# Performance work log

Hardware: AMD Instinct MI355X
Metric: run time of the kernel (lower is better)

## Reference

```python
import jax, jax.numpy as jnp
import numpy as np

LN_EPS = 1e-5

def _mlp3(x, w1, b1, w2, b2, g, bt, w3, b3):
    # Linear -> ReLU -> Linear -> LayerNorm -> ReLU -> Linear
    h = jax.nn.relu(x @ w1 + b1)
    h = h @ w2 + b2
    mu = jnp.mean(h, axis=-1, keepdims=True)
    var = jnp.mean(jnp.square(h - mu), axis=-1, keepdims=True)
    h = g * (h - mu) * jax.lax.rsqrt(var + LN_EPS) + bt
    h = jax.nn.relu(h)
    return h @ w3 + b3

def _edge_index(B, n):
    # fully connected incl. self-loops, row-major (i, j) per graph, batch-offset
    ij = jnp.arange(n * n)
    i = ij // n
    j = ij % n
    off = (jnp.arange(B) * n)[:, None]
    row = (off + i[None, :]).reshape(-1)  # [B*n*n]
    col = (off + j[None, :]).reshape(-1)
    return row, col

def setup_inputs() -> dict:
    key = jax.random.key(0)
    ks = jax.random.split(key, 16)
    D, H = 512, 512
    B, n = 4096, 7
    s = 0.02
    inp = {
        'states': jax.random.normal(ks[0], (B, n, D), jnp.float32),
        'ew1': jax.random.normal(ks[1], (2 * D, H)) * s, 'eb1': jnp.zeros((H,)),
        'ew2': jax.random.normal(ks[2], (H, H)) * s, 'eb2': jnp.zeros((H,)),
        'eg': jnp.ones((H,)), 'ebt': jnp.zeros((H,)),
        'ew3': jax.random.normal(ks[3], (H, H)) * s, 'eb3': jnp.zeros((H,)),
        'nw1': jax.random.normal(ks[4], (D + H, H)) * s, 'nb1': jnp.zeros((H,)),
        'nw2': jax.random.normal(ks[5], (H, H)) * s, 'nb2': jnp.zeros((H,)),
        'ng': jnp.ones((H,)), 'nbt': jnp.zeros((H,)),
        'nw3': jax.random.normal(ks[6], (H, H)) * s, 'nb3': jnp.zeros((H,)),
        'fnw': jax.random.normal(ks[7], (H, 1)) * s, 'fnb': jnp.zeros((1,)),
        'few': jax.random.normal(ks[8], (H, 1)) * s, 'feb': jnp.zeros((1,)),
    }
    return inp

def reference(states, ew1, eb1, ew2, eb2, eg, ebt, ew3, eb3,
              nw1, nb1, nw2, nb2, ng, nbt, nw3, nb3, fnw, fnb, few, feb):
    B, n, D = states.shape
    node = states.reshape(-1, D)                       # [B*n, D]
    row, col = _edge_index(B, n)                       # [B*n*n]

    def edge_mlp(src, tgt):
        return _mlp3(jnp.concatenate([src, tgt], axis=1),
                     ew1, eb1, ew2, eb2, eg, ebt, ew3, eb3)

    edge_attr = edge_mlp(node[row], node[col])         # [B*n*n, H]
    agg = jax.ops.segment_sum(edge_attr, row, num_segments=B * n)
    node2 = _mlp3(jnp.concatenate([node, agg], axis=1),
                  nw1, nb1, nw2, nb2, ng, nbt, nw3, nb3)
    edge_attr2 = edge_mlp(node2[row], node2[col])

    node_out = (node2 @ fnw + fnb).reshape(B, n)       # unary_preds=1
    edge_out = (edge_attr2 @ few + feb).reshape(B, n * n)
    return jnp.concatenate([node_out, edge_out], axis=1)  # [B, n + n*n]
```

## Files before the change

kernel.cpp:

```cpp
#include <hip/hip_runtime.h>

#define LN_EPS 1e-5f

typedef unsigned short u16;
typedef u16 u16x8 __attribute__((ext_vector_type(8)));
typedef __bf16 bf16x8 __attribute__((ext_vector_type(8)));
typedef float f32x4 __attribute__((ext_vector_type(4)));
typedef float f32x2 __attribute__((ext_vector_type(2)));

__device__ __forceinline__ u16 f2bf(float f){
  return __builtin_bit_cast(u16, (__bf16)f);
}
__device__ __forceinline__ float bf2f(u16 b){
  return (float)__builtin_bit_cast(__bf16, b);
}
__device__ __forceinline__ f32x4 mfma16(u16x8 a, u16x8 b, f32x4 c){
  return __builtin_amdgcn_mfma_f32_16x16x32_bf16(
      __builtin_bit_cast(bf16x8, a), __builtin_bit_cast(bf16x8, b), c, 0, 0, 0);
}
__device__ __forceinline__ int uidx(int row, int k){
  return row * 512 + (k ^ ((row & 7) << 3));
}

__device__ __forceinline__ void zero_acc(f32x4 (&acc)[4][4]){
  #pragma unroll
  for (int mt = 0; mt < 4; ++mt)
    #pragma unroll
    for (int ct = 0; ct < 4; ++ct){
      f32x4 z = {0.f, 0.f, 0.f, 0.f};
      acc[mt][ct] = z;
    }
}

__device__ __forceinline__ void preload_b4(const u16* __restrict__ Bp, int wave, int lane,
                                           u16x8 (&b)[4]){
  const u16* bb = Bp + ((size_t)(wave * 4) * 64 + lane) * 8;
  #pragma unroll
  for (int ct = 0; ct < 4; ++ct) b[ct] = *(const u16x8*)&bb[ct * 512];
}

__device__ __forceinline__ void gemm_pipe(const u16* hA, const u16* __restrict__ Bp,
                                          f32x4 (&acc)[4][4], int wave, int lane,
                                          u16x8 (&b_cur)[4]){
  int lrow = lane & 15, lhi = lane >> 4;
  const u16* bb = Bp + ((size_t)(wave * 4) * 64 + lane) * 8;
  u16x8 b_nxt[4], a[4];
  #pragma unroll
  for (int kt = 0; kt < 16; ++kt){
    #pragma unroll
    for (int mt = 0; mt < 4; ++mt)
      a[mt] = *(const u16x8*)&hA[uidx(mt * 16 + lrow, kt * 32 + lhi * 8)];
    if (kt < 15){
      #pragma unroll
      for (int ct = 0; ct < 4; ++ct)
        b_nxt[ct] = *(const u16x8*)&bb[(size_t)(kt + 1) * 16384 + ct * 512];
    }
    __builtin_amdgcn_s_setprio(1);
    #pragma unroll
    for (int ct = 0; ct < 4; ++ct)
      #pragma unroll
      for (int mt = 0; mt < 4; ++mt)
        acc[mt][ct] = mfma16(a[mt], b_cur[ct], acc[mt][ct]);
    __builtin_amdgcn_s_setprio(0);
    #pragma unroll
    for (int ct = 0; ct < 4; ++ct) b_cur[ct] = b_nxt[ct];
  }
}

__device__ __forceinline__ void gemm_k1024_gA(const u16* __restrict__ A0,
                                              const u16* __restrict__ A1, size_t row0,
                                              const u16* __restrict__ Bp,
                                              f32x4 (&acc)[4][4], int wave, int lane){
  int lrow = lane & 15, lhi = lane >> 4;
  const u16* bb = Bp + ((size_t)(wave * 4) * 64 + lane) * 8;
  const u16* a0 = A0 + (row0 + lrow) * 512 + lhi * 8;
  const u16* a1 = A1 + (row0 + lrow) * 512 + lhi * 8;
  u16x8 b_cur[4], b_nxt[4], a[4];
  #pragma unroll
  for (int ct = 0; ct < 4; ++ct) b_cur[ct] = *(const u16x8*)&bb[ct * 512];
  #pragma unroll
  for (int kt = 0; kt < 32; ++kt){
    const u16* ab = (kt < 16) ? a0 : a1;
    int kk = (kt & 15) * 32;
    #pragma unroll
    for (int mt = 0; mt < 4; ++mt)
      a[mt] = *(const u16x8*)&ab[mt * 8192 + kk];
    if (kt < 31){
      #pragma unroll
      for (int ct = 0; ct < 4; ++ct)
        b_nxt[ct] = *(const u16x8*)&bb[(size_t)(kt + 1) * 16384 + ct * 512];
    }
    __builtin_amdgcn_s_setprio(1);
    #pragma unroll
    for (int ct = 0; ct < 4; ++ct)
      #pragma unroll
      for (int mt = 0; mt < 4; ++mt)
        acc[mt][ct] = mfma16(a[mt], b_cur[ct], acc[mt][ct]);
    __builtin_amdgcn_s_setprio(0);
    #pragma unroll
    for (int ct = 0; ct < 4; ++ct) b_cur[ct] = b_nxt[ct];
  }
}

__device__ __forceinline__ void gemm_pipe_s(const u16* hA, const u16* __restrict__ bbBase,
                                            int ktStride, f32x4 (&acc)[4][4],
                                            int lane){
  int lrow = lane & 15, lhi = lane >> 4;
  u16x8 b_cur[4], b_nxt[4], a[4];
  #pragma unroll
  for (int ct = 0; ct < 4; ++ct) b_cur[ct] = *(const u16x8*)&bbBase[ct * 512];
  #pragma unroll
  for (int kt = 0; kt < 16; ++kt){
    #pragma unroll
    for (int mt = 0; mt < 4; ++mt)
      a[mt] = *(const u16x8*)&hA[uidx(mt * 16 + lrow, kt * 32 + lhi * 8)];
    if (kt < 15){
      #pragma unroll
      for (int ct = 0; ct < 4; ++ct)
        b_nxt[ct] = *(const u16x8*)&bbBase[(size_t)(kt + 1) * ktStride + ct * 512];
    }
    __builtin_amdgcn_s_setprio(1);
    #pragma unroll
    for (int ct = 0; ct < 4; ++ct)
      #pragma unroll
      for (int mt = 0; mt < 4; ++mt)
        acc[mt][ct] = mfma16(a[mt], b_cur[ct], acc[mt][ct]);
    __builtin_amdgcn_s_setprio(0);
    #pragma unroll
    for (int ct = 0; ct < 4; ++ct) b_cur[ct] = b_nxt[ct];
  }
}

__device__ __forceinline__ void add_bias8(f32x4 (&acc)[4][4], const float* __restrict__ b,
                                          int wave, int lane){
  int lrow = lane & 15;
  #pragma unroll
  for (int ct = 0; ct < 4; ++ct){
    float bb = b[wave * 64 + ct * 16 + lrow];
    #pragma unroll
    for (int mt = 0; mt < 4; ++mt)
      #pragma unroll
      for (int r = 0; r < 4; ++r) acc[mt][ct][r] += bb;
  }
}

__device__ __forceinline__ void relu_to_lds(f32x4 (&acc)[4][4], u16* hA,
                                            const float* __restrict__ b,
                                            int wave, int lane){
  int lrow = lane & 15, lhi = lane >> 4;
  #pragma unroll
  for (int ct = 0; ct < 4; ++ct){
    int c = wave * 64 + ct * 16 + lrow;
    float bb = b[c];
    #pragma unroll
    for (int mt = 0; mt < 4; ++mt)
      #pragma unroll
      for (int r = 0; r < 4; ++r){
        int row = mt * 16 + lhi * 4 + r;
        hA[uidx(row, c)] = f2bf(fmaxf(acc[mt][ct][r] + bb, 0.f));
      }
  }
}

template<int TO_ACC>
__device__ __forceinline__ void ln_relu8_t(f32x4 (&acc)[4][4], u16* hA,
    f32x2 (*stats)[8], f32x2* mufb,
    const float* __restrict__ b2, const float* __restrict__ g, const float* __restrict__ bt,
    int wave, int lane, int tid)
{
  int lrow = lane & 15, lhi = lane >> 4;
  float s1[4][4], s2[4][4];
  #pragma unroll
  for (int mt = 0; mt < 4; ++mt)
    #pragma unroll
    for (int r = 0; r < 4; ++r){ s1[mt][r] = 0.f; s2[mt][r] = 0.f; }
  #pragma unroll
  for (int ct = 0; ct < 4; ++ct){
    int c = wave * 64 + ct * 16 + lrow;
    float bb = b2[c];
    #pragma unroll
    for (int mt = 0; mt < 4; ++mt)
      #pragma unroll
      for (int r = 0; r < 4; ++r){
        float x = acc[mt][ct][r] + bb;
        acc[mt][ct][r] = x;
        s1[mt][r] += x; s2[mt][r] += x * x;
      }
  }
  #pragma unroll
  for (int off = 1; off < 16; off <<= 1){
    #pragma unroll
    for (int mt = 0; mt < 4; ++mt)
      #pragma unroll
      for (int r = 0; r < 4; ++r){
        s1[mt][r] += __shfl_xor(s1[mt][r], off);
        s2[mt][r] += __shfl_xor(s2[mt][r], off);
      }
  }
  float sa1 = 0.f, sa2 = 0.f;
  #pragma unroll
  for (int mt = 0; mt < 4; ++mt)
    #pragma unroll
    for (int r = 0; r < 4; ++r)
      if (lrow == mt * 4 + r){ sa1 = s1[mt][r]; sa2 = s2[mt][r]; }
  int rowa = (lrow >> 2) * 16 + lhi * 4 + (lrow & 3);
  f32x2 pa = {sa1, sa2};
  stats[rowa][wave] = pa;
  __syncthreads();
  if (tid < 64){
    float a = 0.f, b = 0.f;
    #pragma unroll
    for (int w = 0; w < 8; ++w){ a += stats[tid][w][0]; b += stats[tid][w][1]; }
    float mu  = a * (1.f / 512.f);
    float var = b * (1.f / 512.f) - mu * mu;
    f32x2 mr = {mu, rsqrtf(fmaxf(var, 0.f) + LN_EPS)};
    mufb[tid] = mr;
  }
  __syncthreads();
  float gv[4], btv[4];
  #pragma unroll
  for (int ct = 0; ct < 4; ++ct){
    int c = wave * 64 + ct * 16 + lrow;
    gv[ct] = g[c]; btv[ct] = bt[c];
  }
  #pragma unroll
  for (int mt = 0; mt < 4; ++mt)
    #pragma unroll
    for (int r = 0; r < 4; ++r){
      int row = mt * 16 + lhi * 4 + r;
      f32x2 mr = mufb[row];
      #pragma unroll
      for (int ct = 0; ct < 4; ++ct){
        int c = wave * 64 + ct * 16 + lrow;
        float x = (acc[mt][ct][r] - mr[0]) * mr[1] * gv[ct] + btv[ct];
        if (TO_ACC) acc[mt][ct][r] = fmaxf(x, 0.f);
        else        hA[uidx(row, c)] = f2bf(fmaxf(x, 0.f));
      }
    }
}

__device__ __forceinline__ void head_partial8(f32x4 (&acc)[4][4], const float* __restrict__ w,
                                              f32x2 (*stats)[8], int wave, int lane)
{
  int lrow = lane & 15, lhi = lane >> 4;
  float hs[4][4];
  #pragma unroll
  for (int mt = 0; mt < 4; ++mt)
    #pragma unroll
    for (int r = 0; r < 4; ++r) hs[mt][r] = 0.f;
  #pragma unroll
  for (int ct = 0; ct < 4; ++ct){
    int c = wave * 64 + ct * 16 + lrow;
    float f = w[c];
    #pragma unroll
    for (int mt = 0; mt < 4; ++mt)
      #pragma unroll
      for (int r = 0; r < 4; ++r) hs[mt][r] += acc[mt][ct][r] * f;
  }
  #pragma unroll
  for (int off = 1; off < 16; off <<= 1)
    #pragma unroll
    for (int mt = 0; mt < 4; ++mt)
      #pragma unroll
      for (int r = 0; r < 4; ++r) hs[mt][r] += __shfl_xor(hs[mt][r], off);
  float sa = 0.f;
  #pragma unroll
  for (int mt = 0; mt < 4; ++mt)
    #pragma unroll
    for (int r = 0; r < 4; ++r)
      if (lrow == mt * 4 + r) sa = hs[mt][r];
  int rowa = (lrow >> 2) * 16 + lhi * 4 + (lrow & 3);
  f32x2 pa = {sa, 0.f};
  stats[rowa][wave] = pa;
}

__device__ __forceinline__ void stage_h1(const u16* __restrict__ PQ, int gg, u16* hA,
                                         const float* bias, int wave, int lane){
  const u16* Pg = PQ + (size_t)gg * 7 * 1024;
  u16x8 pA, qA, pB, qB;
  {
    int e = wave;
    int i = e / 7, j = e % 7;
    pA = *(const u16x8*)&Pg[(size_t)i * 1024 + lane * 8];
    qA = *(const u16x8*)&Pg[(size_t)j * 1024 + 512 + lane * 8];
  }
  #pragma unroll
  for (int it = 0; it < 8; ++it){
    int e = it * 8 + wave;
    if (it < 7){
      int e2 = e + 8;
      if (e2 < 49){
        int i = e2 / 7, j = e2 % 7;
        pB = *(const u16x8*)&Pg[(size_t)i * 1024 + lane * 8];
        qB = *(const u16x8*)&Pg[(size_t)j * 1024 + 512 + lane * 8];
      }
    }
    u16x8 o;
    if (e < 49){
      #pragma unroll
      for (int u = 0; u < 8; ++u)
        o[u] = f2bf(fmaxf(bf2f(pA[u]) + bf2f(qA[u]) + bias[u], 0.f));
    } else {
      #pragma unroll
      for (int u = 0; u < 8; ++u) o[u] = 0;
    }
    *(u16x8*)&hA[uidx(e, lane * 8)] = o;
    pA = pB; qA = qB;
  }
}

__global__ __launch_bounds__(512, 2) void edge0_kernel(
    const u16* __restrict__ PQ, const u16* __restrict__ w2p, const u16* __restrict__ w3p,
    const float* __restrict__ b1, const float* __restrict__ b2,
    const float* __restrict__ g, const float* __restrict__ bt, const float* __restrict__ b3,
    u16* __restrict__ agg)
{
  __shared__ alignas(16) u16 hA[64 * 512];
  __shared__ f32x2 stats[64][8];
  __shared__ f32x2 mufb[64];
  int gidx = blockIdx.x;
  int tid = threadIdx.x;
  int wave = tid >> 6, lane = tid & 63;
  int lrow = lane & 15, lhi = lane >> 4;

  const float4* b1v = (const float4*)b1;
  float4 ba = b1v[lane * 2], bb2 = b1v[lane * 2 + 1];
  float bias[8] = {ba.x, ba.y, ba.z, ba.w, bb2.x, bb2.y, bb2.z, bb2.w};

  stage_h1(PQ, gidx, hA, bias, wave, lane);
  u16x8 bpre[4];
  preload_b4(w2p, wave, lane, bpre);
  __syncthreads();

  f32x4 acc[4][4];
  zero_acc(acc);
  gemm_pipe(hA, w2p, acc, wave, lane, bpre);
  ln_relu8_t<0>(acc, hA, stats, mufb, b2, g, bt, wave, lane, tid);
  preload_b4(w3p, wave, lane, bpre);
  __syncthreads();
  {
    int c = tid;
    #pragma unroll
    for (int i = 0; i < 7; ++i){
      float s = 0.f;
      #pragma unroll
      for (int j = 0; j < 7; ++j)
        s += bf2f(hA[uidx(7 * i + j, c)]);
      hA[uidx(49 + i, c)] = f2bf(s);
    }
  }
  __syncthreads();
  f32x4 acc1[4];
  #pragma unroll
  for (int ct = 0; ct < 4; ++ct){ f32x4 z = {0.f,0.f,0.f,0.f}; acc1[ct] = z; }
  {
    const u16* bb = w3p + ((size_t)(wave * 4) * 64 + lane) * 8;
    u16x8 b_nxt[4];
    #pragma unroll
    for (int kt = 0; kt < 16; ++kt){
      u16x8 a0 = *(const u16x8*)&hA[uidx(48 + lrow, kt * 32 + lhi * 8)];
      if (kt < 15){
        #pragma unroll
        for (int ct = 0; ct < 4; ++ct)
          b_nxt[ct] = *(const u16x8*)&bb[(size_t)(kt + 1) * 16384 + ct * 512];
      }
      #pragma unroll
      for (int ct = 0; ct < 4; ++ct)
        acc1[ct] = mfma16(a0, bpre[ct], acc1[ct]);
      #pragma unroll
      for (int ct = 0; ct < 4; ++ct) bpre[ct] = b_nxt[ct];
    }
  }
  #pragma unroll
  for (int ct = 0; ct < 4; ++ct){
    int c = wave * 64 + ct * 16 + lrow;
    float bb3 = 7.f * b3[c];
    #pragma unroll
    for (int r = 0; r < 4; ++r){
      int tr = lhi * 4 + r;
      if (tr >= 1 && tr <= 7){
        int i = tr - 1;
        agg[((size_t)(gidx * 7 + i)) * 512 + c] = f2bf(acc1[ct][r] + bb3);
      }
    }
  }
}

__global__ __launch_bounds__(512, 2) void edge1_kernel(
    const u16* __restrict__ PQ, const u16* __restrict__ w2p,
    const float* __restrict__ b1, const float* __restrict__ b2,
    const float* __restrict__ g, const float* __restrict__ bt,
    const float* __restrict__ w3f, float* __restrict__ out)
{
  __shared__ alignas(16) u16 hA[64 * 512];
  __shared__ f32x2 stats[64][8];
  __shared__ f32x2 mufb[64];
  int gidx = blockIdx.x;
  int tid = threadIdx.x;
  int wave = tid >> 6, lane = tid & 63;

  const float4* b1v = (const float4*)b1;
  float4 ba = b1v[lane * 2], bb2 = b1v[lane * 2 + 1];
  float bias[8] = {ba.x, ba.y, ba.z, ba.w, bb2.x, bb2.y, bb2.z, bb2.w};

  stage_h1(PQ, gidx, hA, bias, wave, lane);
  u16x8 bpre[4];
  preload_b4(w2p, wave, lane, bpre);
  __syncthreads();

  f32x4 acc[4][4];
  zero_acc(acc);
  gemm_pipe(hA, w2p, acc, wave, lane, bpre);
  ln_relu8_t<1>(acc, hA, stats, mufb, b2, g, bt, wave, lane, tid);
  head_partial8(acc, w3f, stats, wave, lane);
  __syncthreads();
  if (tid < 49){
    float s = w3f[512];
    #pragma unroll
    for (int w = 0; w < 8; ++w) s += stats[tid][w][0];
    out[(size_t)gidx * 56 + 7 + tid] = s;
  }
}

__global__ __launch_bounds__(512, 2) void node_mega(
    const u16* __restrict__ nodeb, const u16* __restrict__ aggb,
    const u16* __restrict__ nw1p, const u16* __restrict__ nw2p,
    const u16* __restrict__ nw3p, const u16* __restrict__ w1p,
    const float* __restrict__ nb1, const float* __restrict__ nb2,
    const float* __restrict__ ng, const float* __restrict__ nbt,
    const float* __restrict__ nb3, const float* __restrict__ hw,
    const float* __restrict__ hb,
    u16* __restrict__ PQ, float* __restrict__ out)
{
  __shared__ alignas(16) u16 hA[64 * 512];
  __shared__ f32x2 stats[64][8];
  __shared__ f32x2 mufb[64];
  int tid = threadIdx.x;
  int wave = tid >> 6, lane = tid & 63;
  int lrow = lane & 15, lhi = lane >> 4;
  size_t row0 = (size_t)blockIdx.x * 64;

  f32x4 acc[4][4];
  zero_acc(acc);
  gemm_k1024_gA(nodeb, aggb, row0, nw1p, acc, wave, lane);
  relu_to_lds(acc, hA, nb1, wave, lane);
  u16x8 bpre[4];
  preload_b4(nw2p, wave, lane, bpre);
  __syncthreads();
  zero_acc(acc);
  gemm_pipe(hA, nw2p, acc, wave, lane, bpre);
  ln_relu8_t<0>(acc, hA, stats, mufb, nb2, ng, nbt, wave, lane, tid);
  preload_b4(nw3p, wave, lane, bpre);
  __syncthreads();
  zero_acc(acc);
  gemm_pipe(hA, nw3p, acc, wave, lane, bpre);
  add_bias8(acc, nb3, wave, lane);
  __syncthreads();
  #pragma unroll
  for (int ct = 0; ct < 4; ++ct){
    int c = wave * 64 + ct * 16 + lrow;
    #pragma unroll
    for (int mt = 0; mt < 4; ++mt)
      #pragma unroll
      for (int r = 0; r < 4; ++r)
        hA[uidx(mt * 16 + lhi * 4 + r, c)] = f2bf(acc[mt][ct][r]);
  }
  head_partial8(acc, hw, stats, wave, lane);
  __syncthreads();
  if (tid < 64){
    size_t v = row0 + tid;
    float s = hb[0];
    #pragma unroll
    for (int w = 0; w < 8; ++w) s += stats[tid][w][0];
    out[(v / 7) * 56 + (v % 7)] = s;
  }
  #pragma unroll
  for (int p = 0; p < 2; ++p){
    zero_acc(acc);
    const u16* bbBase = w1p + (((size_t)(p * 32) + wave * 4) * 64 + lane) * 8;
    gemm_pipe_s(hA, bbBase, 32768, acc, lane);
    #pragma unroll
    for (int ct = 0; ct < 4; ++ct){
      int c = p * 512 + wave * 64 + ct * 16 + lrow;
      #pragma unroll
      for (int mt = 0; mt < 4; ++mt)
        #pragma unroll
        for (int r = 0; r < 4; ++r){
          size_t grow = row0 + mt * 16 + lhi * 4 + r;
          PQ[grow * 1024 + c] = f2bf(acc[mt][ct][r]);
        }
    }
  }
}

__global__ __launch_bounds__(256, 2) void gemm64_0(
    const u16* __restrict__ A0, const u16* __restrict__ Bp, u16* __restrict__ Cout)
{
  int tid = threadIdx.x;
  int wave = tid >> 6, lane = tid & 63;
  int lrow = lane & 15, lhi = lane >> 4;
  size_t row0 = (size_t)blockIdx.x * 64;
  int coff = blockIdx.y * 512;
  const u16* bb = Bp + (((size_t)(coff >> 4) + wave * 8) * 64 + lane) * 8;
  f32x4 acc[4][8];
  #pragma unroll
  for (int mt = 0; mt < 4; ++mt)
    #pragma unroll
    for (int ct = 0; ct < 8; ++ct){
      f32x4 z = {0.f, 0.f, 0.f, 0.f};
      acc[mt][ct] = z;
    }
  u16x8 b_cur[8], b_nxt[8];
  #pragma unroll
  for (int ct = 0; ct < 8; ++ct) b_cur[ct] = *(const u16x8*)&bb[ct * 512];
  #pragma unroll
  for (int kt = 0; kt < 16; ++kt){
    u16x8 af[4];
    #pragma unroll
    for (int mt = 0; mt < 4; ++mt)
      af[mt] = *(const u16x8*)&A0[(row0 + mt * 16 + lrow) * 512 + kt * 32 + lhi * 8];
    if (kt < 15){
      #pragma unroll
      for (int ct = 0; ct < 8; ++ct)
        b_nxt[ct] = *(const u16x8*)&bb[((size_t)(kt + 1) * 64 * 64 + ct * 64) * 8];
    }
    __builtin_amdgcn_s_setprio(1);
    #pragma unroll
    for (int ct = 0; ct < 8; ++ct)
      #pragma unroll
      for (int mt = 0; mt < 4; ++mt) acc[mt][ct] = mfma16(af[mt], b_cur[ct], acc[mt][ct]);
    __builtin_amdgcn_s_setprio(0);
    #pragma unroll
    for (int ct = 0; ct < 8; ++ct) b_cur[ct] = b_nxt[ct];
  }
  #pragma unroll
  for (int ct = 0; ct < 8; ++ct){
    int c = coff + wave * 128 + ct * 16 + lrow;
    #pragma unroll
    for (int mt = 0; mt < 4; ++mt)
      #pragma unroll
      for (int r = 0; r < 4; ++r){
        size_t grow = row0 + mt * 16 + lhi * 4 + r;
        Cout[grow * 1024 + c] = f2bf(acc[mt][ct][r]);
      }
  }
}

__global__ void fold_w3(const float* __restrict__ W3, const float* __restrict__ hw,
                        const float* __restrict__ b3, const float* __restrict__ hb,
                        float* __restrict__ w3f)
{
  int k = blockIdx.x, l = threadIdx.x;
  const float* row = (k < 512) ? (W3 + (size_t)k * 512) : b3;
  float s = 0.f;
  for (int c = l; c < 512; c += 64) s += row[c] * hw[c];
  #pragma unroll
  for (int off = 32; off; off >>= 1) s += __shfl_down(s, off);
  if (l == 0) w3f[k] = (k < 512) ? s : s + hb[0];
}

__global__ void pack_w(const float* __restrict__ W, u16* __restrict__ dst,
                       int K, int N, int w1mode)
{
  int idx = blockIdx.x * 256 + threadIdx.x;
  int total = (K >> 5) * (N >> 4) * 64;
  if (idx >= total) return;
  int lane = idx & 63;
  int t = idx >> 6;
  int nt = N >> 4;
  int ct = t % nt;
  int kt = t / nt;
  int c  = ct * 16 + (lane & 15);
  int k0 = kt * 32 + (lane >> 4) * 8;
  u16x8 o;
  #pragma unroll
  for (int j = 0; j < 8; ++j){
    int k = k0 + j;
    float v;
    if (w1mode){
      v = (c < 512) ? W[(size_t)k * 512 + c] : W[(size_t)(k + 512) * 512 + (c - 512)];
    } else {
      v = W[(size_t)k * N + c];
    }
    o[j] = f2bf(v);
  }
  *(u16x8*)&dst[(size_t)idx * 8] = o;
}

__global__ void cast_node(const float* __restrict__ src, u16* __restrict__ dst, int n8){
  int idx = blockIdx.x * 256 + threadIdx.x;
  if (idx >= n8) return;
  const float4* s = (const float4*)src;
  float4 a = s[(size_t)idx * 2], b = s[(size_t)idx * 2 + 1];
  u16x8 o;
  o[0] = f2bf(a.x); o[1] = f2bf(a.y); o[2] = f2bf(a.z); o[3] = f2bf(a.w);
  o[4] = f2bf(b.x); o[5] = f2bf(b.y); o[6] = f2bf(b.z); o[7] = f2bf(b.w);
  *(u16x8*)&dst[(size_t)idx * 8] = o;
}

extern "C" void kernel_launch(void* const* d_in, const int* in_sizes, int n_in,
                              void* d_out, int out_size, void* d_ws, size_t ws_size,
                              hipStream_t stream)
{
  (void)in_sizes; (void)n_in; (void)out_size; (void)ws_size;
  const float* states = (const float*)d_in[0];
  const float* ew1 = (const float*)d_in[1];
  const float* eb1 = (const float*)d_in[2];
  const float* ew2 = (const float*)d_in[3];
  const float* eb2 = (const float*)d_in[4];
  const float* eg  = (const float*)d_in[5];
  const float* ebt = (const float*)d_in[6];
  const float* ew3 = (const float*)d_in[7];
  const float* eb3 = (const float*)d_in[8];
  const float* nw1 = (const float*)d_in[9];
  const float* nb1 = (const float*)d_in[10];
  const float* nw2 = (const float*)d_in[11];
  const float* nb2 = (const float*)d_in[12];
  const float* ng  = (const float*)d_in[13];
  const float* nbt = (const float*)d_in[14];
  const float* nw3 = (const float*)d_in[15];
  const float* nb3 = (const float*)d_in[16];
  const float* fnw = (const float*)d_in[17];
  const float* fnb = (const float*)d_in[18];
  const float* few = (const float*)d_in[19];
  const float* feb = (const float*)d_in[20];
  float* out = (float*)d_out;

  char* ws = (char*)d_ws;
  size_t off = 0;
  auto alloc = [&](size_t bytes) -> void* {
    void* p = ws + off;
    off += (bytes + 255) & ~(size_t)255;
    return p;
  };
  const size_t NV = 28672;
  u16* PQ    = (u16*)alloc(NV * 1024 * 2);
  u16* nodeb = (u16*)alloc(NV * 512 * 2);
  u16* aggb  = (u16*)alloc(NV * 512 * 2);
  u16* w1p   = (u16*)alloc(512 * 1024 * 2);
  u16* nw1p  = (u16*)alloc(1024 * 512 * 2);
  u16* w2p   = (u16*)alloc(512 * 512 * 2);
  u16* w3p   = (u16*)alloc(512 * 512 * 2);
  u16* nw2p  = (u16*)alloc(512 * 512 * 2);
  u16* nw3p  = (u16*)alloc(512 * 512 * 2);
  float* w3f = (float*)alloc(513 * 4);

  pack_w<<<256, 256, 0, stream>>>(ew1, w1p, 512, 1024, 1);
  pack_w<<<256, 256, 0, stream>>>(nw1, nw1p, 1024, 512, 0);
  pack_w<<<128, 256, 0, stream>>>(ew2, w2p, 512, 512, 0);
  pack_w<<<128, 256, 0, stream>>>(ew3, w3p, 512, 512, 0);
  pack_w<<<128, 256, 0, stream>>>(nw2, nw2p, 512, 512, 0);
  pack_w<<<128, 256, 0, stream>>>(nw3, nw3p, 512, 512, 0);
  fold_w3<<<513, 64, 0, stream>>>(ew3, few, eb3, feb, w3f);
  cast_node<<<7168, 256, 0, stream>>>(states, nodeb, (int)(NV * 512 / 8));

  gemm64_0<<<dim3(448, 2), 256, 0, stream>>>(nodeb, w1p, PQ);
  edge0_kernel<<<4096, 512, 0, stream>>>(PQ, w2p, w3p, eb1, eb2, eg, ebt, eb3, aggb);
  node_mega<<<448, 512, 0, stream>>>(nodeb, aggb, nw1p, nw2p, nw3p, w1p,
                                     nb1, nb2, ng, nbt, nb3, fnw, fnb, PQ, out);
  edge1_kernel<<<4096, 512, 0, stream>>>(PQ, w2p, eb1, eb2, eg, ebt, w3f, out);
}
```

Baseline: 592.7 us.

## Fold edge W3 into node W1 so edge0 emits summed hidden rows

Uses linearity: agg = sum_j(h_j) @ eW3 + 7*eb3, so agg @ nW1b equals hsum @ (eW3 @ nW1b) plus a constant bias. The edge0 kernel now writes only the per-node sums of the post-LN hidden rows and drops its small W3 GEMM. A precomputed fused weight (eW3·nW1b, formed by a small GEMM) and a folded bias replace it in the node MLP. This removes per-graph MFMA work and weight loads from edge0, but adds per-call weight-prep kernels and a different bf16 rounding path.

```diff
diff --git a/kernel.cpp b/kernel.cpp
--- a/kernel.cpp
+++ b/kernel.cpp
@@ -310,10 +310,10 @@
 }
 
 __global__ __launch_bounds__(512, 2) void edge0_kernel(
-    const u16* __restrict__ PQ, const u16* __restrict__ w2p, const u16* __restrict__ w3p,
+    const u16* __restrict__ PQ, const u16* __restrict__ w2p,
     const float* __restrict__ b1, const float* __restrict__ b2,
-    const float* __restrict__ g, const float* __restrict__ bt, const float* __restrict__ b3,
-    u16* __restrict__ agg)
+    const float* __restrict__ g, const float* __restrict__ bt,
+    u16* __restrict__ hsum)
 {
   __shared__ alignas(16) u16 hA[64 * 512];
   __shared__ f32x2 stats[64][8];
@@ -321,7 +321,6 @@
   int gidx = blockIdx.x;
   int tid = threadIdx.x;
   int wave = tid >> 6, lane = tid & 63;
-  int lrow = lane & 15, lhi = lane >> 4;
 
   const float4* b1v = (const float4*)b1;
   float4 ba = b1v[lane * 2], bb2 = b1v[lane * 2 + 1];
@@ -336,7 +335,6 @@
   zero_acc(acc);
   gemm_pipe(hA, w2p, acc, wave, lane, bpre);
   ln_relu8_t<0>(acc, hA, stats, mufb, b2, g, bt, wave, lane, tid);
-  preload_b4(w3p, wave, lane, bpre);
   __syncthreads();
   {
     int c = tid;
@@ -346,42 +344,7 @@
       #pragma unroll
       for (int j = 0; j < 7; ++j)
         s += bf2f(hA[uidx(7 * i + j, c)]);
-      hA[uidx(49 + i, c)] = f2bf(s);
-    }
-  }
-  __syncthreads();
-  f32x4 acc1[4];
-  #pragma unroll
-  for (int ct = 0; ct < 4; ++ct){ f32x4 z = {0.f,0.f,0.f,0.f}; acc1[ct] = z; }
-  {
-    const u16* bb = w3p + ((size_t)(wave * 4) * 64 + lane) * 8;
-    u16x8 b_nxt[4];
-    #pragma unroll
-    for (int kt = 0; kt < 16; ++kt){
-      u16x8 a0 = *(const u16x8*)&hA[uidx(48 + lrow, kt * 32 + lhi * 8)];
-      if (kt < 15){
-        #pragma unroll
-        for (int ct = 0; ct < 4; ++ct)
-          b_nxt[ct] = *(const u16x8*)&bb[(size_t)(kt + 1) * 16384 + ct * 512];
-      }
-      #pragma unroll
-      for (int ct = 0; ct < 4; ++ct)
-        acc1[ct] = mfma16(a0, bpre[ct], acc1[ct]);
-      #pragma unroll
-      for (int ct = 0; ct < 4; ++ct) bpre[ct] = b_nxt[ct];
-    }
-  }
-  #pragma unroll
-  for (int ct = 0; ct < 4; ++ct){
-    int c = wave * 64 + ct * 16 + lrow;
-    float bb3 = 7.f * b3[c];
-    #pragma unroll
-    for (int r = 0; r < 4; ++r){
-      int tr = lhi * 4 + r;
-      if (tr >= 1 && tr <= 7){
-        int i = tr - 1;
-        agg[((size_t)(gidx * 7 + i)) * 512 + c] = f2bf(acc1[ct][r] + bb3);
-      }
+      hsum[((size_t)(gidx * 7 + i)) * 512 + c] = f2bf(s);
     }
   }
 }
@@ -423,10 +386,10 @@
 }
 
 __global__ __launch_bounds__(512, 2) void node_mega(
-    const u16* __restrict__ nodeb, const u16* __restrict__ aggb,
-    const u16* __restrict__ nw1p, const u16* __restrict__ nw2p,
+    const u16* __restrict__ nodeb, const u16* __restrict__ hsumb,
+    const u16* __restrict__ nw1cat, const u16* __restrict__ nw2p,
     const u16* __restrict__ nw3p, const u16* __restrict__ w1p,
-    const float* __restrict__ nb1, const float* __restrict__ nb2,
+    const float* __restrict__ bvec, const float* __restrict__ nb2,
     const float* __restrict__ ng, const float* __restrict__ nbt,
     const float* __restrict__ nb3, const float* __restrict__ hw,
     const float* __restrict__ hb,
@@ -442,8 +405,8 @@
 
   f32x4 acc[4][4];
   zero_acc(acc);
-  gemm_k1024_gA(nodeb, aggb, row0, nw1p, acc, wave, lane);
-  relu_to_lds(acc, hA, nb1, wave, lane);
+  gemm_k1024_gA(nodeb, hsumb, row0, nw1cat, acc, wave, lane);
+  relu_to_lds(acc, hA, bvec, wave, lane);
   u16x8 bpre[4];
   preload_b4(nw2p, wave, lane, bpre);
   __syncthreads();
@@ -544,6 +507,64 @@
         Cout[grow * 1024 + c] = f2bf(acc[mt][ct][r]);
       }
   }
+}
+
+__global__ __launch_bounds__(256) void gemm_w3n(
+    const float* __restrict__ A, const u16* __restrict__ Bp, float* __restrict__ C)
+{
+  int tid = threadIdx.x;
+  int wave = tid >> 6, lane = tid & 63;
+  int lrow = lane & 15, lhi = lane >> 4;
+  size_t row0 = (size_t)blockIdx.x * 64;
+  const u16* bb = Bp + (((size_t)(wave * 8)) * 64 + lane) * 8;
+  f32x4 acc[4][8];
+  #pragma unroll
+  for (int mt = 0; mt < 4; ++mt)
+    #pragma unroll
+    for (int ct = 0; ct < 8; ++ct){
+      f32x4 z = {0.f, 0.f, 0.f, 0.f};
+      acc[mt][ct] = z;
+    }
+  for (int kt = 0; kt < 16; ++kt){
+    u16x8 af[4], bv[8];
+    #pragma unroll
+    for (int mt = 0; mt < 4; ++mt){
+      const float* ar = A + (row0 + mt * 16 + lrow) * 512 + kt * 32 + lhi * 8;
+      float4 v0 = *(const float4*)ar, v1 = *(const float4*)(ar + 4);
+      af[mt][0] = f2bf(v0.x); af[mt][1] = f2bf(v0.y);
+      af[mt][2] = f2bf(v0.z); af[mt][3] = f2bf(v0.w);
+      af[mt][4] = f2bf(v1.x); af[mt][5] = f2bf(v1.y);
+      af[mt][6] = f2bf(v1.z); af[mt][7] = f2bf(v1.w);
+    }
+    #pragma unroll
+    for (int ct = 0; ct < 8; ++ct)
+      bv[ct] = *(const u16x8*)&bb[(size_t)kt * 16384 + ct * 512];
+    #pragma unroll
+    for (int ct = 0; ct < 8; ++ct)
+      #pragma unroll
+      for (int mt = 0; mt < 4; ++mt) acc[mt][ct] = mfma16(af[mt], bv[ct], acc[mt][ct]);
+  }
+  #pragma unroll
+  for (int ct = 0; ct < 8; ++ct){
+    int c = wave * 128 + ct * 16 + lrow;
+    #pragma unroll
+    for (int mt = 0; mt < 4; ++mt)
+      #pragma unroll
+      for (int r = 0; r < 4; ++r){
+        size_t grow = row0 + mt * 16 + lhi * 4 + r;
+        C[grow * 512 + c] = acc[mt][ct][r];
+      }
+  }
+}
+
+__global__ void fold_bvec(const float* __restrict__ nb1, const float* __restrict__ b3,
+                          const float* __restrict__ nw1, float* __restrict__ bvec)
+{
+  int c = threadIdx.x;
+  float s = 0.f;
+  for (int m = 0; m < 512; ++m)
+    s += b3[m] * nw1[(size_t)(512 + m) * 512 + c];
+  bvec[c] = nb1[c] + 7.f * s;
 }
 
 __global__ void fold_w3(const float* __restrict__ W3, const float* __restrict__ hw,
@@ -634,29 +655,34 @@
     return p;
   };
   const size_t NV = 28672;
-  u16* PQ    = (u16*)alloc(NV * 1024 * 2);
-  u16* nodeb = (u16*)alloc(NV * 512 * 2);
-  u16* aggb  = (u16*)alloc(NV * 512 * 2);
-  u16* w1p   = (u16*)alloc(512 * 1024 * 2);
-  u16* nw1p  = (u16*)alloc(1024 * 512 * 2);
-  u16* w2p   = (u16*)alloc(512 * 512 * 2);
-  u16* w3p   = (u16*)alloc(512 * 512 * 2);
-  u16* nw2p  = (u16*)alloc(512 * 512 * 2);
-  u16* nw3p  = (u16*)alloc(512 * 512 * 2);
-  float* w3f = (float*)alloc(513 * 4);
+  u16* PQ     = (u16*)alloc(NV * 1024 * 2);
+  u16* nodeb  = (u16*)alloc(NV * 512 * 2);
+  u16* hsumb  = (u16*)alloc(NV * 512 * 2);
+  u16* w1p    = (u16*)alloc(512 * 1024 * 2);
+  u16* nw1cat = (u16*)alloc(1024 * 512 * 2);
+  u16* nw1bp  = (u16*)alloc(512 * 512 * 2);
+  u16* w2p    = (u16*)alloc(512 * 512 * 2);
+  u16* nw2p   = (u16*)alloc(512 * 512 * 2);
+  u16* nw3p   = (u16*)alloc(512 * 512 * 2);
+  float* w3n  = (float*)alloc(512 * 512 * 4);
+  float* w3f  = (float*)alloc(513 * 4);
+  float* bvec = (float*)alloc(512 * 4);
 
   pack_w<<<256, 256, 0, stream>>>(ew1, w1p, 512, 1024, 1);
-  pack_w<<<256, 256, 0, stream>>>(nw1, nw1p, 1024, 512, 0);
+  pack_w<<<128, 256, 0, stream>>>(nw1, nw1cat, 512, 512, 0);
+  pack_w<<<128, 256, 0, stream>>>(nw1 + 512 * 512, nw1bp, 512, 512, 0);
   pack_w<<<128, 256, 0, stream>>>(ew2, w2p, 512, 512, 0);
-  pack_w<<<128, 256, 0, stream>>>(ew3, w3p, 512, 512, 0);
   pack_w<<<128, 256, 0, stream>>>(nw2, nw2p, 512, 512, 0);
   pack_w<<<128, 256, 0, stream>>>(nw3, nw3p, 512, 512, 0);
   fold_w3<<<513, 64, 0, stream>>>(ew3, few, eb3, feb, w3f);
+  fold_bvec<<<1, 512, 0, stream>>>(nb1, eb3, nw1, bvec);
+  gemm_w3n<<<8, 256, 0, stream>>>(ew3, nw1bp, w3n);
+  pack_w<<<128, 256, 0, stream>>>(w3n, nw1cat + 512 * 512, 512, 512, 0);
   cast_node<<<7168, 256, 0, stream>>>(states, nodeb, (int)(NV * 512 / 8));
 
   gemm64_0<<<dim3(448, 2), 256, 0, stream>>>(nodeb, w1p, PQ);
-  edge0_kernel<<<4096, 512, 0, stream>>>(PQ, w2p, w3p, eb1, eb2, eg, ebt, eb3, aggb);
-  node_mega<<<448, 512, 0, stream>>>(nodeb, aggb, nw1p, nw2p, nw3p, w1p,
-                                     nb1, nb2, ng, nbt, nb3, fnw, fnb, PQ, out);
+  edge0_kernel<<<4096, 512, 0, stream>>>(PQ, w2p, eb1, eb2, eg, ebt, hsumb);
+  node_mega<<<448, 512, 0, stream>>>(nodeb, hsumb, nw1cat, nw2p, nw3p, w1p,
+                                     bvec, nb2, ng, nbt, nb3, fnw, fnb, PQ, out);
   edge1_kernel<<<4096, 512, 0, stream>>>(PQ, w2p, eb1, eb2, eg, ebt, w3f, out);
 }
```

Result: faster. 580.3 us (-2.1%).
